# Kernel optimization log

Hardware: AMD Instinct MI355X
Metric: run time of the kernel (lower is better)

## Reference

```python
import jax, jax.numpy as jnp
import numpy as np

B, IMG_DIM, H, W = 2, 256, 64, 64
PC_C, PC_D = 16, 16          # voxel_dim = PC_C * PC_D = 256
VOXEL_DIM = PC_C * PC_D
QK_DIM = 256                 # out_channels of img_conv / voxel_conv


def _conv1x1(x, w, b):
    # x: [B, Cin, H, W], w: [Cout, Cin], b: [Cout]  (1x1 conv == per-pixel matmul)
    return jnp.einsum('bchw,oc->bohw', x, w) + b[None, :, None, None]


def setup_inputs() -> dict:
    key = jax.random.key(0)
    ks = jax.random.split(key, 10)
    s = 0.02
    return {
        'img': jax.random.normal(ks[0], (B, IMG_DIM, H, W), jnp.float32),
        'pc': jax.random.normal(ks[1], (B, PC_D, H, W, PC_C), jnp.float32),  # dense() layout [B,D,H,W,C]
        'img_conv_w': jax.random.normal(ks[2], (QK_DIM, IMG_DIM), jnp.float32) * s,
        'img_conv_b': jnp.zeros((QK_DIM,), jnp.float32),
        'voxel_conv_w': jax.random.normal(ks[3], (QK_DIM, VOXEL_DIM), jnp.float32) * s,
        'voxel_conv_b': jnp.zeros((QK_DIM,), jnp.float32),
        'img_v_w': jax.random.normal(ks[4], (IMG_DIM, IMG_DIM), jnp.float32) * s,
        'img_v_b': jnp.zeros((IMG_DIM,), jnp.float32),
        'voxel_v_w': jax.random.normal(ks[5], (VOXEL_DIM, VOXEL_DIM), jnp.float32) * s,
        'voxel_v_b': jnp.zeros((VOXEL_DIM,), jnp.float32),
    }


def reference(img, pc, img_conv_w, img_conv_b, voxel_conv_w, voxel_conv_b,
              img_v_w, img_v_b, voxel_v_w, voxel_v_b):
    b, c_img, h, w = img.shape
    # pc.dense() -> permute(0,4,1,2,3) -> [B, C, D, H, W] -> [B, C*D, H, W]
    pc = jnp.transpose(pc, (0, 4, 1, 2, 3))
    pcb, pcc, pcd, pch, pcw = pc.shape
    pc2 = pc.reshape(pcb, pcc * pcd, pch, pcw)
    n = h * w  # == pch * pcw (required by the bmms)

    img_q = _conv1x1(img, img_conv_w, img_conv_b).reshape(b, QK_DIM, n).transpose(0, 2, 1)  # [B, N, 256]
    pc_k = _conv1x1(pc2, voxel_conv_w, voxel_conv_b).reshape(b, QK_DIM, n)                  # [B, 256, N]
    # unscaled single-head cross attention, softmax over voxel positions
    attn = jax.nn.softmax(jnp.einsum('bnc,bcm->bnm', img_q, pc_k), axis=-1)                 # [B, N_img, N_pc]

    img_v = _conv1x1(img, img_v_w, img_v_b).reshape(b, c_img, n)                            # [B, C_img, N]
    img_v = jnp.einsum('bcn,bmn->bcm', img_v, attn).reshape(b, c_img, h, w)                 # img_v @ attn^T

    pc_v = _conv1x1(pc2, voxel_v_w, voxel_v_b).reshape(b, pcc * pcd, n)                     # [B, C*D, N]
    pc_v = jnp.einsum('bcn,bmn->bcm', pc_v, attn).reshape(b, pcc, pcd, pch, pcw)
    return (img_v, pc_v)
```

## Files before the change

kernel.cpp:

```cpp
#include <hip/hip_runtime.h>
#include <hip/hip_bf16.h>


typedef __hip_bfloat16 bf16;
typedef __attribute__((ext_vector_type(8))) short bf16x8;
typedef __attribute__((ext_vector_type(4))) float f32x4;

#define AS1 __attribute__((address_space(1)))
#define AS3 __attribute__((address_space(3)))

__device__ __forceinline__ void gld_lds16(const bf16* g, bf16* s) {
    __builtin_amdgcn_global_load_lds((const AS1 void*)g, (AS3 void*)s, 16, 0, 0);
}

__device__ __forceinline__ bf16x8 cvt8(const float* __restrict__ p) {
    const float4 a = *(const float4*)p;
    const float4 b = *(const float4*)(p + 4);
    bf16 t[8];
    t[0] = __float2bfloat16(a.x); t[1] = __float2bfloat16(a.y);
    t[2] = __float2bfloat16(a.z); t[3] = __float2bfloat16(a.w);
    t[4] = __float2bfloat16(b.x); t[5] = __float2bfloat16(b.y);
    t[6] = __float2bfloat16(b.z); t[7] = __float2bfloat16(b.w);
    return *(const bf16x8*)t;
}

__global__ __launch_bounds__(256) void proj_kernel(
    const float* __restrict__ img, const float* __restrict__ pc,
    const float* __restrict__ Wq,  const float* __restrict__ bq,
    const float* __restrict__ Wk,  const float* __restrict__ bk,
    const float* __restrict__ Wvi, const float* __restrict__ bvi,
    const float* __restrict__ Wvp, const float* __restrict__ bvp,
    bf16* __restrict__ Qw, bf16* __restrict__ Ktw, bf16* __restrict__ Vall)
{
    __shared__ __align__(16) bf16 XT[64][264];

    const int blk = blockIdx.x;
    const int s   = blk >> 8;
    const int b   = (blk >> 7) & 1;
    const int g   = (blk >> 6) & 1;
    const int n0  = (blk & 63) * 64;
    const int tid = threadIdx.x;

    if (s == 0) {
        const float* src = img + b * 1048576;
        for (int k = 0; k < 16; k++) {
            const int i = tid + k * 256;
            const int cin = i >> 4, nl4 = (i & 15) * 4;
            const float4 v = *(const float4*)&src[cin * 4096 + n0 + nl4];
            XT[nl4 + 0][cin] = __float2bfloat16(v.x);
            XT[nl4 + 1][cin] = __float2bfloat16(v.y);
            XT[nl4 + 2][cin] = __float2bfloat16(v.z);
            XT[nl4 + 3][cin] = __float2bfloat16(v.w);
        }
    } else {
        const float* src = pc + b * 1048576;
        for (int k = 0; k < 16; k++) {
            const int d = k, u = tid;
            const int nl = u >> 2, c4 = (u & 3) * 4;
            const float4 v = *(const float4*)&src[d * 65536 + (n0 + nl) * 16 + c4];
            XT[nl][(c4 + 0) * 16 + d] = __float2bfloat16(v.x);
            XT[nl][(c4 + 1) * 16 + d] = __float2bfloat16(v.y);
            XT[nl][(c4 + 2) * 16 + d] = __float2bfloat16(v.z);
            XT[nl][(c4 + 3) * 16 + d] = __float2bfloat16(v.w);
        }
    }
    __syncthreads();

    const float* W = s ? (g ? Wvp : Wk) : (g ? Wvi : Wq);
    const float* Bv = s ? (g ? bvp : bk) : (g ? bvi : bq);

    const int wv = tid >> 6, lane = tid & 63, l16 = lane & 15, quad = lane >> 4;
    const int ob = wv * 64;

    f32x4 acc[4][4] = {};

    for (int ks = 0; ks < 8; ks++) {
        const int k0 = ks * 32;
        bf16x8 af[4], wf[4];
        for (int ti = 0; ti < 4; ti++)
            af[ti] = *(const bf16x8*)&XT[ti * 16 + l16][k0 + quad * 8];
        for (int tj = 0; tj < 4; tj++)
            wf[tj] = cvt8(&W[(ob + tj * 16 + l16) * 256 + k0 + quad * 8]);
        for (int ti = 0; ti < 4; ti++)
            for (int tj = 0; tj < 4; tj++)
                acc[ti][tj] = __builtin_amdgcn_mfma_f32_16x16x32_bf16(af[ti], wf[tj], acc[ti][tj], 0, 0, 0);
    }

    if (g == 0) {
        bf16* D1 = (s ? Ktw : Qw) + b * (4096 * 256);
        for (int tj = 0; tj < 4; tj++) {
            const int o = ob + tj * 16 + l16;
            const float bias = Bv[o];
            for (int ti = 0; ti < 4; ti++) {
                const int nl = ti * 16 + quad * 4;
                for (int r = 0; r < 4; r++)
                    D1[(n0 + nl + r) * 256 + o] = __float2bfloat16(acc[ti][tj][r] + bias);
            }
        }
    } else {
        bf16* D2 = Vall + b * (512 * 4096) + (s ? 256 * 4096 : 0);
        for (int tj = 0; tj < 4; tj++) {
            const int o = ob + tj * 16 + l16;
            const float bias = Bv[o];
            for (int ti = 0; ti < 4; ti++) {
                const int nl = ti * 16 + quad * 4;
                bf16 pv[4];
                for (int r = 0; r < 4; r++)
                    pv[r] = __float2bfloat16(acc[ti][tj][r] + bias);
                *(uint2*)&D2[o * 4096 + n0 + nl] = *(const uint2*)pv;
            }
        }
    }
}

__global__ __launch_bounds__(256) void attn_s_kernel(
    const bf16* __restrict__ Qw, const bf16* __restrict__ Ktw,
    bf16* __restrict__ Pt, float* __restrict__ Lpart)
{
    __shared__ __align__(16) bf16 As[128 * 32];
    __shared__ __align__(16) bf16 Bs[128 * 32];

    const int b  = blockIdx.z;
    const int q0 = blockIdx.y * 128;
    const int p0 = blockIdx.x * 128;
    const bf16* A = Qw  + b * (4096 * 256);
    const bf16* B = Ktw + b * (4096 * 256);

    const int tid = threadIdx.x;
    const int wv = tid >> 6, lane = tid & 63, l16 = lane & 15, quad = lane >> 4;
    const int wr = wv >> 1, wc = wv & 1;

    f32x4 acc[4][4] = {};

    for (int ks = 0; ks < 8; ks++) {
        const int k0 = ks * 32;
        bf16x8 av[2], bv[2];
        for (int c = 0; c < 2; c++) {
            const int ci = c * 256 + tid;
            const int row = ci >> 2, kc = ci & 3;
            av[c] = *(const bf16x8*)&A[(q0 + row) * 256 + k0 + kc * 8];
            bv[c] = *(const bf16x8*)&B[(p0 + row) * 256 + k0 + kc * 8];
        }
        __syncthreads();
        for (int c = 0; c < 2; c++) {
            const int ci = c * 256 + tid;
            *(bf16x8*)&As[ci * 8] = av[c];
            *(bf16x8*)&Bs[ci * 8] = bv[c];
        }
        __syncthreads();
        bf16x8 af[4], bfr[4];
        for (int t = 0; t < 4; t++) {
            af[t]  = *(const bf16x8*)&As[(wr * 64 + t * 16 + l16) * 32 + quad * 8];
            bfr[t] = *(const bf16x8*)&Bs[(wc * 64 + t * 16 + l16) * 32 + quad * 8];
        }
        for (int ti = 0; ti < 4; ti++)
            for (int tj = 0; tj < 4; tj++)
                acc[ti][tj] = __builtin_amdgcn_mfma_f32_16x16x32_bf16(af[ti], bfr[tj], acc[ti][tj], 0, 0, 0);
    }

    bf16* Pdst = Pt + (size_t)b * 4096 * 4096;
    const int strip = blockIdx.x * 2 + wc;
    for (int ti = 0; ti < 4; ti++) {
        for (int r = 0; r < 4; r++) {
            const int qrow = wr * 64 + ti * 16 + quad * 4 + r;
            const int q = q0 + qrow;
            float partial = 0.0f;
            for (int tj = 0; tj < 4; tj++) {
                const float e = __expf(fminf(acc[ti][tj][r], 80.0f));
                partial += e;
                Pdst[(size_t)q * 4096 + p0 + wc * 64 + tj * 16 + l16] = __float2bfloat16(e);
            }
            partial += __shfl_xor(partial, 1);
            partial += __shfl_xor(partial, 2);
            partial += __shfl_xor(partial, 4);
            partial += __shfl_xor(partial, 8);
            if (l16 == 0)
                Lpart[(size_t)(b * 4096 + q) * 64 + strip] = partial;
        }
    }
}

__global__ __launch_bounds__(256) void lred_kernel(
    const float* __restrict__ Lpart, float* __restrict__ Linv)
{
    const int row = blockIdx.x * 256 + threadIdx.x;
    const float4* lp = (const float4*)&Lpart[(size_t)row * 64];
    float s = 0.0f;
    for (int i = 0; i < 16; i++) {
        const float4 v = lp[i];
        s += v.x + v.y + v.z + v.w;
    }
    Linv[row] = 1.0f / fmaxf(s, 1e-30f);
}

__global__ __launch_bounds__(512, 4) void attn_o_kernel(
    const bf16* __restrict__ Vall, const bf16* __restrict__ Pt,
    const float* __restrict__ Linv, float* __restrict__ out)
{
    __shared__ __align__(16) bf16 smem[2][2][6144];

    const int b  = blockIdx.z;
    const int c0 = blockIdx.y * 128;
    const int q0 = blockIdx.x * 64;
    const bf16* A = Vall + (size_t)b * 512 * 4096;
    const bf16* B = Pt   + (size_t)b * 4096 * 4096;

    const int tid = threadIdx.x;
    const int grp = tid >> 8;
    const int t8  = tid & 255;
    const int wv = t8 >> 6, lane = t8 & 63, l16 = lane & 15, quad = lane >> 4;
    const int wr = wv >> 1, wc = wv & 1;

    int aoff[4], boff[2];
    for (int t = 0; t < 4; t++) {
        const int row = wr * 64 + t * 16 + l16;
        aoff[t] = row * 32 + (quad ^ ((row >> 1) & 3)) * 8;
    }
    for (int t = 0; t < 2; t++) {
        const int row = wc * 32 + t * 16 + l16;
        boff[t] = row * 32 + (quad ^ ((row >> 1) & 3)) * 8;
    }

    const int arow = t8 >> 2;
    const int kswz = ((t8 & 3) ^ ((arow >> 1) & 3)) * 8;
    const bf16* Ag0 = A + (c0 + arow) * 4096 + grp * 2048 + kswz;
    const bf16* Ag1 = A + (c0 + 64 + arow) * 4096 + grp * 2048 + kswz;
    const bf16* Bg  = B + (q0 + arow) * 4096 + grp * 2048 + kswz;

    f32x4 acc[4][2] = {};

#define STAGE(buf, ks)                                                  \
    do {                                                                \
        const int _k = (ks) * 32;                                       \
        bf16* _s = &smem[grp][(buf)][0];                                \
        gld_lds16(Ag0 + _k, _s + t8 * 8);                               \
        gld_lds16(Ag1 + _k, _s + 2048 + t8 * 8);                        \
        gld_lds16(Bg  + _k, _s + 4096 + t8 * 8);                        \
    } while (0)

    STAGE(0, 0);
    int cur = 0;
    for (int ks = 0; ks < 64; ks++) {
        if (ks + 1 < 64) {
            STAGE(cur ^ 1, ks + 1);
            asm volatile("s_waitcnt vmcnt(3)" ::: "memory");
        } else {
            asm volatile("s_waitcnt vmcnt(0)" ::: "memory");
        }
        __builtin_amdgcn_s_barrier();
        __builtin_amdgcn_sched_barrier(0);

        const bf16* As_ = &smem[grp][cur][0];
        const bf16* Bs_ = &smem[grp][cur][4096];
        bf16x8 af[4], bfr[2];
        for (int t = 0; t < 4; t++) af[t]  = *(const bf16x8*)&As_[aoff[t]];
        for (int t = 0; t < 2; t++) bfr[t] = *(const bf16x8*)&Bs_[boff[t]];
        __builtin_amdgcn_s_setprio(1);
        for (int ti = 0; ti < 4; ti++)
            for (int tj = 0; tj < 2; tj++)
                acc[ti][tj] = __builtin_amdgcn_mfma_f32_16x16x32_bf16(af[ti], bfr[tj], acc[ti][tj], 0, 0, 0);
        __builtin_amdgcn_s_setprio(0);

        asm volatile("s_waitcnt lgkmcnt(0)" ::: "memory");
        __builtin_amdgcn_s_barrier();
        cur ^= 1;
    }
#undef STAGE

    __syncthreads();

    float* comb = (float*)&smem[0][0];
    const int sl0 = (wr * 64 + quad * 4) * 64 + wc * 32 + l16;
    if (grp == 0) {
        for (int ti = 0; ti < 4; ti++)
            for (int tj = 0; tj < 2; tj++)
                for (int r = 0; r < 4; r++)
                    comb[sl0 + (ti * 16 + r) * 64 + tj * 16] = acc[ti][tj][r];
    }
    __syncthreads();
    if (grp == 1) {
        for (int ti = 0; ti < 4; ti++)
            for (int tj = 0; tj < 2; tj++)
                for (int r = 0; r < 4; r++)
                    comb[sl0 + (ti * 16 + r) * 64 + tj * 16] += acc[ti][tj][r];
    }
    __syncthreads();

    const int f0 = tid * 16;
    const int cl = f0 >> 6, ql = f0 & 63;
    const int c_ = c0 + cl;
    const size_t base = (c_ < 256)
        ? ((size_t)b * 1048576 + (size_t)c_ * 4096)
        : (2097152u + (size_t)b * 1048576 + (size_t)(c_ - 256) * 4096);
    for (int j = 0; j < 4; j++) {
        const float4 v = *(const float4*)&comb[f0 + j * 4];
        const float4 l = *(const float4*)&Linv[b * 4096 + q0 + ql + j * 4];
        float4 o;
        o.x = v.x * l.x; o.y = v.y * l.y; o.z = v.z * l.z; o.w = v.w * l.w;
        *(float4*)&out[base + q0 + ql + j * 4] = o;
    }
}

extern "C" void kernel_launch(void* const* d_in, const int* in_sizes, int n_in,
                              void* d_out, int out_size, void* d_ws, size_t ws_size,
                              hipStream_t stream)
{
    const float* img = (const float*)d_in[0];
    const float* pc  = (const float*)d_in[1];
    const float* Wq  = (const float*)d_in[2];
    const float* bq  = (const float*)d_in[3];
    const float* Wk  = (const float*)d_in[4];
    const float* bk  = (const float*)d_in[5];
    const float* Wvi = (const float*)d_in[6];
    const float* bvi = (const float*)d_in[7];
    const float* Wvp = (const float*)d_in[8];
    const float* bvp = (const float*)d_in[9];

    char* ws = (char*)d_ws;
    bf16*  Qw    = (bf16*)(ws);
    bf16*  Ktw   = (bf16*)(ws + (4ull  << 20));
    bf16*  Vall  = (bf16*)(ws + (8ull  << 20));
    bf16*  Pt    = (bf16*)(ws + (16ull << 20));
    float* Lpart = (float*)(ws + (80ull << 20));
    float* Linv  = (float*)(ws + (82ull << 20));

    proj_kernel<<<512, 256, 0, stream>>>(img, pc, Wq, bq, Wk, bk,
                                         Wvi, bvi, Wvp, bvp, Qw, Ktw, Vall);
    attn_s_kernel<<<dim3(32, 32, 2), 256, 0, stream>>>(Qw, Ktw, Pt, Lpart);
    lred_kernel<<<32, 256, 0, stream>>>(Lpart, Linv);
    attn_o_kernel<<<dim3(64, 4, 2), 512, 0, stream>>>(Vall, Pt, Linv, (float*)d_out);
}
```

Baseline: 202.3 us.

## Pipeline score GEMM with async LDS loads, swizzle, and vectorized P stores

Reworks the attention-score kernel to double-buffer the Q and K tiles in LDS, loading them with global_load_lds and waiting with explicit vmcnt counts so the next tile's load overlaps the current MFMAs. The LDS layout is XOR-swizzled to avoid bank conflicts, and MFMA priority is raised with setprio. The operand roles are swapped so each lane holds four consecutive P columns, which turns the scalar bf16 writes of the exp'd scores into 8-byte vector stores and changes the row-sum reduction to cross-quad shuffles. Occupancy is hinted at 4 blocks per CU, and LDS use doubles.

```diff
diff --git a/kernel.cpp b/kernel.cpp
--- a/kernel.cpp
+++ b/kernel.cpp
@@ -113,70 +113,97 @@
     }
 }
 
-__global__ __launch_bounds__(256) void attn_s_kernel(
+__global__ __launch_bounds__(256, 4) void attn_s_kernel(
     const bf16* __restrict__ Qw, const bf16* __restrict__ Ktw,
     bf16* __restrict__ Pt, float* __restrict__ Lpart)
 {
-    __shared__ __align__(16) bf16 As[128 * 32];
-    __shared__ __align__(16) bf16 Bs[128 * 32];
+    __shared__ __align__(16) bf16 smem[2][8192];
 
     const int b  = blockIdx.z;
     const int q0 = blockIdx.y * 128;
     const int p0 = blockIdx.x * 128;
-    const bf16* A = Qw  + b * (4096 * 256);
-    const bf16* B = Ktw + b * (4096 * 256);
+    const bf16* Aq = Qw  + b * (4096 * 256);
+    const bf16* Ak = Ktw + b * (4096 * 256);
 
     const int tid = threadIdx.x;
     const int wv = tid >> 6, lane = tid & 63, l16 = lane & 15, quad = lane >> 4;
     const int wr = wv >> 1, wc = wv & 1;
 
+    int aoff[4], boff[4];
+    for (int t = 0; t < 4; t++) {
+        const int rowa = wr * 64 + t * 16 + l16;
+        aoff[t] = rowa * 32 + (quad ^ ((rowa >> 1) & 3)) * 8;
+        const int rowb = wc * 64 + t * 16 + l16;
+        boff[t] = rowb * 32 + (quad ^ ((rowb >> 1) & 3)) * 8;
+    }
+
+    const int arow0 = tid >> 2;
+    const int kswz = ((tid & 3) ^ ((arow0 >> 1) & 3)) * 8;
+    const bf16* Ag0 = Ak + (p0 + arow0) * 256 + kswz;
+    const bf16* Ag1 = Ak + (p0 + 64 + arow0) * 256 + kswz;
+    const bf16* Bg0 = Aq + (q0 + arow0) * 256 + kswz;
+    const bf16* Bg1 = Aq + (q0 + 64 + arow0) * 256 + kswz;
+
     f32x4 acc[4][4] = {};
 
+#define SSTAGE(buf, ks)                                                 \
+    do {                                                                \
+        const int _k = (ks) * 32;                                       \
+        bf16* _s = &smem[(buf)][0];                                     \
+        gld_lds16(Ag0 + _k, _s + tid * 8);                              \
+        gld_lds16(Ag1 + _k, _s + 2048 + tid * 8);                       \
+        gld_lds16(Bg0 + _k, _s + 4096 + tid * 8);                       \
+        gld_lds16(Bg1 + _k, _s + 6144 + tid * 8);                       \
+    } while (0)
+
+    SSTAGE(0, 0);
+    int cur = 0;
     for (int ks = 0; ks < 8; ks++) {
-        const int k0 = ks * 32;
-        bf16x8 av[2], bv[2];
-        for (int c = 0; c < 2; c++) {
-            const int ci = c * 256 + tid;
-            const int row = ci >> 2, kc = ci & 3;
-            av[c] = *(const bf16x8*)&A[(q0 + row) * 256 + k0 + kc * 8];
-            bv[c] = *(const bf16x8*)&B[(p0 + row) * 256 + k0 + kc * 8];
-        }
-        __syncthreads();
-        for (int c = 0; c < 2; c++) {
-            const int ci = c * 256 + tid;
-            *(bf16x8*)&As[ci * 8] = av[c];
-            *(bf16x8*)&Bs[ci * 8] = bv[c];
-        }
-        __syncthreads();
+        if (ks + 1 < 8) {
+            SSTAGE(cur ^ 1, ks + 1);
+            asm volatile("s_waitcnt vmcnt(4)" ::: "memory");
+        } else {
+            asm volatile("s_waitcnt vmcnt(0)" ::: "memory");
+        }
+        __builtin_amdgcn_s_barrier();
+        __builtin_amdgcn_sched_barrier(0);
+
+        const bf16* As_ = &smem[cur][0];
+        const bf16* Bs_ = &smem[cur][4096];
         bf16x8 af[4], bfr[4];
-        for (int t = 0; t < 4; t++) {
-            af[t]  = *(const bf16x8*)&As[(wr * 64 + t * 16 + l16) * 32 + quad * 8];
-            bfr[t] = *(const bf16x8*)&Bs[(wc * 64 + t * 16 + l16) * 32 + quad * 8];
-        }
+        for (int t = 0; t < 4; t++) af[t]  = *(const bf16x8*)&As_[aoff[t]];
+        for (int t = 0; t < 4; t++) bfr[t] = *(const bf16x8*)&Bs_[boff[t]];
+        __builtin_amdgcn_s_setprio(1);
         for (int ti = 0; ti < 4; ti++)
             for (int tj = 0; tj < 4; tj++)
                 acc[ti][tj] = __builtin_amdgcn_mfma_f32_16x16x32_bf16(af[ti], bfr[tj], acc[ti][tj], 0, 0, 0);
-    }
+        __builtin_amdgcn_s_setprio(0);
+
+        asm volatile("s_waitcnt lgkmcnt(0)" ::: "memory");
+        __builtin_amdgcn_s_barrier();
+        cur ^= 1;
+    }
+#undef SSTAGE
 
     bf16* Pdst = Pt + (size_t)b * 4096 * 4096;
-    const int strip = blockIdx.x * 2 + wc;
-    for (int ti = 0; ti < 4; ti++) {
-        for (int r = 0; r < 4; r++) {
-            const int qrow = wr * 64 + ti * 16 + quad * 4 + r;
-            const int q = q0 + qrow;
-            float partial = 0.0f;
-            for (int tj = 0; tj < 4; tj++) {
+    const int strip = blockIdx.x * 2 + wr;
+    for (int tj = 0; tj < 4; tj++) {
+        const int q = q0 + wc * 64 + tj * 16 + l16;
+        float partial = 0.0f;
+        for (int ti = 0; ti < 4; ti++) {
+            const int p = p0 + wr * 64 + ti * 16 + quad * 4;
+            bf16 pv[4];
+            for (int r = 0; r < 4; r++) {
                 const float e = __expf(fminf(acc[ti][tj][r], 80.0f));
                 partial += e;
-                Pdst[(size_t)q * 4096 + p0 + wc * 64 + tj * 16 + l16] = __float2bfloat16(e);
+                pv[r] = __float2bfloat16(e);
             }
-            partial += __shfl_xor(partial, 1);
-            partial += __shfl_xor(partial, 2);
-            partial += __shfl_xor(partial, 4);
-            partial += __shfl_xor(partial, 8);
-            if (l16 == 0)
-                Lpart[(size_t)(b * 4096 + q) * 64 + strip] = partial;
-        }
+            *(uint2*)&Pdst[(size_t)q * 4096 + p] = *(const uint2*)pv;
+        }
+        partial += __shfl_xor(partial, 16);
+        partial += __shfl_xor(partial, 32);
+        if (lane < 16)
+            Lpart[(size_t)(b * 4096 + q) * 64 + strip] = partial;
     }
 }
 
```

After: 199.4 us. About the same (-1.4%).
